# Performance work log

Hardware: AMD Instinct MI355X
Metric: run time of the kernel (lower is better)

Reference implementation:

```python
import jax, jax.numpy as jnp
import numpy as np

NUM_HEADS = 16
HEAD_DIM = 64
HIDDEN = 1024
ROPE_BASE = 10000.0


def _rope_cache(seq_len, dtype):
    inv_freq = 1.0 / (ROPE_BASE ** (jnp.arange(0, HEAD_DIM, 2, dtype=jnp.float32) / HEAD_DIM))
    freqs = jnp.arange(seq_len, dtype=jnp.float32)[:, None] * inv_freq[None, :]  # [S, D/2]
    emb = jnp.concatenate([freqs, freqs], axis=-1)  # [S, D]
    return jnp.cos(emb).astype(dtype), jnp.sin(emb).astype(dtype)


def _rotate_half(x):
    x1, x2 = jnp.split(x, 2, axis=-1)
    return jnp.concatenate([-x2, x1], axis=-1)


def setup_inputs() -> dict:
    key = jax.random.key(0)
    k1, k2, k3 = jax.random.split(key, 3)
    B, S = 1, 4096
    x = jax.random.normal(k1, (B, S, HIDDEN), dtype=jnp.float32)
    w_qkv = jax.random.normal(k2, (3 * HIDDEN, HIDDEN), dtype=jnp.float32) * (1.0 / np.sqrt(HIDDEN))
    w_out = jax.random.normal(k3, (HIDDEN, HIDDEN), dtype=jnp.float32) * (1.0 / np.sqrt(HIDDEN))
    return {"x": x, "w_qkv": w_qkv, "w_out": w_out}


def reference(x, w_qkv, w_out):
    B, S, _ = x.shape
    scale = 1.0 / np.sqrt(HEAD_DIM)
    # fused QKV projection (torch Linear: x @ W^T)
    qkv = jnp.einsum('bsd,ed->bse', x, w_qkv)
    qkv = qkv.reshape(B, S, 3, NUM_HEADS, HEAD_DIM).transpose(2, 0, 3, 1, 4)
    q, k, v = qkv[0], qkv[1], qkv[2]  # [B, H, S, Dh]
    cos, sin = _rope_cache(S, x.dtype)  # [S, Dh]
    cos = cos[None, None]
    sin = sin[None, None]
    q = q * cos + _rotate_half(q) * sin
    k = k * cos + _rotate_half(k) * sin
    scores = jnp.einsum('bhqd,bhkd->bhqk', q, k) * scale  # [B, H, S, S]
    causal = jnp.triu(jnp.ones((S, S), dtype=bool), k=1)
    min_val = jnp.finfo(scores.dtype).min
    scores = jnp.where(causal[None, None], min_val, scores)
    attn = jax.nn.softmax(scores, axis=-1)
    out = jnp.einsum('bhqk,bhkd->bhqd', attn, v)  # [B, H, S, Dh]
    out = out.transpose(0, 2, 1, 3).reshape(B, S, HIDDEN)
    return jnp.einsum('bsd,ed->bse', out, w_out)
```

## Files before the change

kernel.cpp:

```cpp
#include <hip/hip_runtime.h>

#define S_LEN 4096
#define NHEAD 16
#define DHEAD 64
#define HID 1024

typedef float f32x4 __attribute__((ext_vector_type(4)));
typedef float f32x16 __attribute__((ext_vector_type(16)));
typedef unsigned short u16x8 __attribute__((ext_vector_type(8)));
typedef __bf16 bf16x8 __attribute__((ext_vector_type(8)));

__device__ __forceinline__ unsigned short f2bf(float f) {
  union { float f; unsigned u; } x; x.f = f;
  return (unsigned short)((x.u + 0x7FFFu + ((x.u >> 16) & 1u)) >> 16);
}
__device__ __forceinline__ float bf2f(unsigned short u) {
  union { unsigned u; float f; } x; x.u = ((unsigned)u) << 16;
  return x.f;
}
__device__ __forceinline__ f32x4 mfma16(u16x8 a, u16x8 b, f32x4 c) {
  return __builtin_amdgcn_mfma_f32_16x16x32_bf16(
      __builtin_bit_cast(bf16x8, a), __builtin_bit_cast(bf16x8, b), c, 0, 0, 0);
}
__device__ __forceinline__ f32x16 mfma32(u16x8 a, u16x8 b, f32x16 c) {
  return __builtin_amdgcn_mfma_f32_32x32x16_bf16(
      __builtin_bit_cast(bf16x8, a), __builtin_bit_cast(bf16x8, b), c, 0, 0, 0);
}
__device__ __forceinline__ void gload16(const void* g, void* l) {
  __builtin_amdgcn_global_load_lds(
      (const __attribute__((address_space(1))) void*)g,
      (__attribute__((address_space(3))) void*)l, 16, 0, 0);
}
__device__ __forceinline__ void permswap(unsigned& a, unsigned& b) {
#if __has_builtin(__builtin_amdgcn_permlane32_swap)
  typedef unsigned u32x2 __attribute__((ext_vector_type(2)));
  u32x2 r = __builtin_amdgcn_permlane32_swap(a, b, false, false);
  a = r[0]; b = r[1];
#else
  asm volatile("v_permlane32_swap_b32 %0, %1" : "+v"(a), "+v"(b));
#endif
}
__device__ __forceinline__ unsigned cvtpk(float lo, float hi) {
  unsigned r;
  asm("v_cvt_pk_bf16_f32 %0, %1, %2" : "=v"(r) : "v"(lo), "v"(hi));
  return r;
}
__device__ __forceinline__ float fexp2(float x) {
  float r;
  asm("v_exp_f32 %0, %1" : "=v"(r) : "v"(x));
  return r;
}

__global__ void k_cvt_all(const float4* __restrict__ x, const float4* __restrict__ wq,
                          const float4* __restrict__ wo, ushort4* __restrict__ xb,
                          ushort4* __restrict__ wqb, ushort4* __restrict__ wob) {
  int i = blockIdx.x * blockDim.x + threadIdx.x;
  const float4* src; ushort4* dst; int off;
  if (i < 1048576)      { src = x;  dst = xb;  off = i; }
  else if (i < 1835008) { src = wq; dst = wqb; off = i - 1048576; }
  else                  { src = wo; dst = wob; off = i - 1835008; }
  float4 v = src[off];
  ushort4 o;
  o.x = f2bf(v.x); o.y = f2bf(v.y); o.z = f2bf(v.z); o.w = f2bf(v.w);
  dst[off] = o;
}

__global__ void k_rope_split(const unsigned short* __restrict__ qkv,
                             unsigned short* __restrict__ Q,
                             unsigned short* __restrict__ Kf) {
  int s = blockIdx.x;
  int t = threadIdx.x;
  int h = t >> 5, i = t & 31;
  float inv = fexp2(-(float)i * 0.4152410118609203f);
  float ang = (float)s * inv;
  float sn, cs;
  __sincosf(ang, &sn, &cs);
  const unsigned short* row = qkv + (size_t)s * 3072;
  float q1 = bf2f(row[h * 64 + i]);
  float q2 = bf2f(row[h * 64 + i + 32]);
  float k1 = bf2f(row[1024 + h * 64 + i]);
  float k2 = bf2f(row[1024 + h * 64 + i + 32]);
  const float ksc = 0.125f * 1.44269504f;
  size_t qo = ((size_t)h * S_LEN + s) * 64 + i;
  Q[qo]      = f2bf(q1 * cs - q2 * sn);
  Q[qo + 32] = f2bf(q2 * cs + q1 * sn);
  int t32 = s >> 5, kv = s & 31;
  size_t ko = ((((size_t)h * 128 + t32) * 4 + (i >> 4)) * 2 + ((i >> 3) & 1)) * 256 + kv * 8 + (i & 7);
  Kf[ko]        = f2bf((k1 * cs - k2 * sn) * ksc);
  Kf[ko + 1024] = f2bf((k2 * cs + k1 * sn) * ksc);
}

__global__ void k_vt(const unsigned short* __restrict__ qkv,
                     unsigned short* __restrict__ Vf) {
  __shared__ unsigned short tile[64][65];
  int st = blockIdx.x, h = blockIdx.y;
  int t = threadIdx.x;
  int r = t >> 2, c0 = (t & 3) * 16;
  const unsigned short* src = qkv + (size_t)(st * 64 + r) * 3072 + 2048 + h * 64 + c0;
  u16x8 a = *(const u16x8*)src;
  u16x8 b = *(const u16x8*)(src + 8);
#pragma unroll
  for (int j = 0; j < 8; ++j) { tile[r][c0 + j] = a[j]; tile[r][c0 + 8 + j] = b[j]; }
  __syncthreads();
#pragma unroll
  for (int pass = 0; pass < 2; ++pass) {
    int task = t + pass * 256;
    int o = task >> 6, d = task & 63;
    int t32 = st * 2 + (o >> 2), kc = (o >> 1) & 1, hfv = o & 1;
    u16x8 v;
#pragma unroll
    for (int e = 0; e < 8; ++e) v[e] = tile[o * 8 + e][d];
    *(u16x8*)(Vf + (((((size_t)h * 128 + t32) * 2 + kc) * 2 + hfv) * 64 + d) * 8) = v;
  }
}

__device__ __forceinline__ void stc(float* p, float v) { *p = v; }
__device__ __forceinline__ void stc(unsigned short* p, float v) { *p = f2bf(v); }

template <typename OutT>
__global__ __launch_bounds__(256) void gemm_bt(
    const unsigned short* __restrict__ A, const unsigned short* __restrict__ B,
    OutT* __restrict__ C, int M, int N, int K) {
  __shared__ __attribute__((aligned(16))) unsigned short As[2][128][64];
  __shared__ __attribute__((aligned(16))) unsigned short Bs[2][128][64];
  const int tid = threadIdx.x;
  const int w = tid >> 6, lane = tid & 63;
  const int bm = blockIdx.y * 128, bn = blockIdx.x * 128;
  const int wr = w >> 1, wc = w & 1;
  const int l8 = lane >> 3;
  const int c8 = (lane & 7) * 8;
  f32x4 acc[4][4] = {};

  auto stage = [&](int buf, int k0) {
#pragma unroll
    for (int c = 0; c < 4; ++c) {
      int row = w * 32 + c * 8;
      gload16(A + (size_t)(bm + row + l8) * K + k0 + c8, &As[buf][row][0]);
      gload16(B + (size_t)(bn + row + l8) * K + k0 + c8, &Bs[buf][row][0]);
    }
  };

  const int nk = K >> 6;
  stage(0, 0);
  int cur = 0;
  for (int kt = 0; kt < nk; ++kt) {
    __syncthreads();
    if (kt + 1 < nk) stage(cur ^ 1, (kt + 1) << 6);
#pragma unroll
    for (int kk = 0; kk < 2; ++kk) {
      u16x8 af[4], bfr[4];
#pragma unroll
      for (int m = 0; m < 4; ++m)
        af[m] = *(const u16x8*)&As[cur][wr * 64 + m * 16 + (lane & 15)][kk * 32 + (lane >> 4) * 8];
#pragma unroll
      for (int n = 0; n < 4; ++n)
        bfr[n] = *(const u16x8*)&Bs[cur][wc * 64 + n * 16 + (lane & 15)][kk * 32 + (lane >> 4) * 8];
#pragma unroll
      for (int m = 0; m < 4; ++m)
#pragma unroll
        for (int n = 0; n < 4; ++n)
          acc[m][n] = mfma16(af[m], bfr[n], acc[m][n]);
    }
    cur ^= 1;
  }
#pragma unroll
  for (int m = 0; m < 4; ++m) {
    int row = bm + wr * 64 + m * 16 + (lane >> 4) * 4;
#pragma unroll
    for (int n = 0; n < 4; ++n) {
      int col = bn + wc * 64 + n * 16 + (lane & 15);
#pragma unroll
      for (int j = 0; j < 4; ++j) stc(&C[(size_t)(row + j) * N + col], acc[m][n][j]);
    }
  }
}

__device__ __forceinline__ void attn_tile(
    const unsigned short* __restrict__ Q,
    const unsigned short* __restrict__ kfb,
    const unsigned short* __restrict__ vfb,
    unsigned short* __restrict__ O,
    char* eb, int h, int qt, int w, int q31, int hf) {
  const int qb = qt * 128;
  const int qg = qb + w * 32 + q31;

  u16x8 qf[4];
  {
    const unsigned short* qp = Q + ((size_t)h * S_LEN + qg) * 64 + hf * 8;
#pragma unroll
    for (int c = 0; c < 4; ++c) qf[c] = *(const u16x8*)(qp + c * 16);
  }

  f32x16 accA = {}, accB = {};
  float l_own = 0.f;

  const int kOffBase = hf * 256 + q31 * 8;
  const int vOffBase = hf * 512 + q31 * 8;
  const int nst = qt * 4 + w + 1;

  u16x8 ka[4], kb_[4], kc2[4], va[4], vb_[4], vc2[4];
#define LOADK(dst, t)                                                         \
  {                                                                           \
    const unsigned short* p_ = kfb + (size_t)(t) * 2048 + kOffBase;           \
    dst[0] = *(const u16x8*)(p_);                                             \
    dst[1] = *(const u16x8*)(p_ + 512);                                       \
    dst[2] = *(const u16x8*)(p_ + 1024);                                      \
    dst[3] = *(const u16x8*)(p_ + 1536);                                      \
  }
#define LOADV(dst, t)                                                         \
  {                                                                           \
    const unsigned short* p_ = vfb + (size_t)(t) * 2048 + vOffBase;           \
    dst[0] = *(const u16x8*)(p_);                                             \
    dst[1] = *(const u16x8*)(p_ + 256);                                       \
    dst[2] = *(const u16x8*)(p_ + 1024);                                      \
    dst[3] = *(const u16x8*)(p_ + 1280);                                      \
  }
#define STEP(t, kc_, vc_, kn_, vn_)                                           \
  {                                                                           \
    const int tn = ((t) + 2 < nst) ? (t) + 2 : nst - 1;                       \
    LOADK(kn_, tn);                                                           \
    LOADV(vn_, tn);                                                           \
    f32x16 sc = {};                                                           \
    __builtin_amdgcn_s_setprio(1);                                            \
    _Pragma("unroll") for (int c = 0; c < 4; ++c) sc = mfma32(kc_[c], qf[c], sc); \
    __builtin_amdgcn_s_setprio(0);                                            \
    if ((t) == nst - 1) {                     \
      _Pragma("unroll") for (int r = 0; r < 16; ++r) {                        \
        int kvl = (t) * 32 + (r & 3) + 8 * (r >> 2) + 4 * hf;                 \
        if (kvl > qg) sc[r] = -1e30f;                                         \
      }                                                                       \
    }                                                                         \
    float p[16];                                                              \
    _Pragma("unroll") for (int r = 0; r < 16; ++r) p[r] = fexp2(sc[r]);       \
    l_own += (((p[0] + p[1]) + (p[2] + p[3])) + ((p[4] + p[5]) + (p[6] + p[7]))) + \
             (((p[8] + p[9]) + (p[10] + p[11])) + ((p[12] + p[13]) + (p[14] + p[15]))); \
    unsigned dw[8];                                                           \
    _Pragma("unroll") for (int k = 0; k < 8; ++k) dw[k] = cvtpk(p[2 * k], p[2 * k + 1]); \
    __builtin_amdgcn_s_setprio(1);                                            \
    _Pragma("unroll") for (int kc = 0; kc < 2; ++kc) {                        \
      unsigned x0 = dw[4 * kc + 0], x1 = dw[4 * kc + 1];                      \
      unsigned y0 = dw[4 * kc + 2], y1 = dw[4 * kc + 3];                      \
      permswap(x0, y0);                                                       \
      permswap(x1, y1);                                                       \
      union { u16x8 v; unsigned u[4]; } pf;                                   \
      pf.u[0] = x0; pf.u[1] = x1; pf.u[2] = y0; pf.u[3] = y1;                 \
      accA = mfma32(vc_[kc * 2 + 0], pf.v, accA);                             \
      accB = mfma32(vc_[kc * 2 + 1], pf.v, accB);                             \
    }                                                                         \
    __builtin_amdgcn_s_setprio(0);                                            \
  }

  {
    const int t1 = (1 < nst) ? 1 : nst - 1;
    LOADK(ka, 0);
    LOADV(va, 0);
    LOADK(kb_, t1);
    LOADV(vb_, t1);
  }
  int t = 0;
  while (true) {
    STEP(t, ka, va, kc2, vc2);
    if (++t >= nst) break;
    STEP(t, kb_, vb_, ka, va);
    if (++t >= nst) break;
    STEP(t, kc2, vc2, kb_, vb_);
    if (++t >= nst) break;
  }
#undef STEP
#undef LOADK
#undef LOADV

  float l_run;
  {
    unsigned a = __float_as_uint(l_own), b = a;
    permswap(a, b);
    l_run = __uint_as_float(a) + __uint_as_float(b);
  }
  const float inv = 1.0f / l_run;
#pragma unroll
  for (int dblk = 0; dblk < 2; ++dblk) {
#pragma unroll
    for (int tt = 0; tt < 4; ++tt) {
      float a0, a1, a2, a3;
      if (dblk == 0) { a0 = accA[4 * tt]; a1 = accA[4 * tt + 1]; a2 = accA[4 * tt + 2]; a3 = accA[4 * tt + 3]; }
      else           { a0 = accB[4 * tt]; a1 = accB[4 * tt + 1]; a2 = accB[4 * tt + 2]; a3 = accB[4 * tt + 3]; }
      unsigned d0 = cvtpk(a0 * inv, a1 * inv);
      unsigned d1 = cvtpk(a2 * inv, a3 * inv);
      int dbase = dblk * 32 + 8 * tt + 4 * hf;
      int off = (q31 * 128 + dbase * 2) ^ ((q31 & 7) << 4);
      *(uint2*)(eb + off) = make_uint2(d0, d1);
    }
  }
  const int lane = hf * 32 + q31;
#pragma unroll
  for (int pass = 0; pass < 4; ++pass) {
    int q = (lane >> 3) + pass * 8;
    int c8 = lane & 7;
    u16x8 vv = *(const u16x8*)(eb + ((q * 128 + c8 * 16) ^ ((q & 7) << 4)));
    *(u16x8*)(O + (size_t)(qb + w * 32 + q) * HID + h * 64 + c8 * 8) = vv;
  }
}

__global__ __launch_bounds__(256) void flash_attn(
    const unsigned short* __restrict__ Q,
    const unsigned short* __restrict__ Kf,
    const unsigned short* __restrict__ Vf,
    unsigned short* __restrict__ O) {
  __shared__ __attribute__((aligned(16))) unsigned short ebuf[4][2048];
  const int tid = threadIdx.x;
  const int w = tid >> 6, lane = tid & 63;
  const int q31 = lane & 31, hf = lane >> 5;
  const int h = blockIdx.x;
  const int p = blockIdx.y;
  const unsigned short* kfb = Kf + (size_t)h * 128 * 2048;
  const unsigned short* vfb = Vf + (size_t)h * 128 * 2048;
  char* eb = (char*)&ebuf[w][0];
  attn_tile(Q, kfb, vfb, O, eb, h, p, w, q31, hf);
  attn_tile(Q, kfb, vfb, O, eb, h, 31 - p, w, q31, hf);
}

extern "C" void kernel_launch(void* const* d_in, const int* in_sizes, int n_in,
                              void* d_out, int out_size, void* d_ws, size_t ws_size,
                              hipStream_t stream) {
  const float* x = (const float*)d_in[0];
  const float* w_qkv = (const float*)d_in[1];
  const float* w_out = (const float*)d_in[2];
  float* out = (float*)d_out;
  char* ws = (char*)d_ws;

  unsigned short* xb    = (unsigned short*)(ws + 0);
  unsigned short* wqkvb = (unsigned short*)(ws + 8388608);
  unsigned short* woutb = (unsigned short*)(ws + 14680064);
  unsigned short* qkvb  = (unsigned short*)(ws + 16777216);
  unsigned short* Qb    = (unsigned short*)(ws + 41943040);
  unsigned short* Kfb   = (unsigned short*)(ws + 50331648);
  unsigned short* Vfb   = (unsigned short*)(ws + 58720256);
  unsigned short* attnb = (unsigned short*)(ws + 67108864);

  k_cvt_all<<<dim3(8192), dim3(256), 0, stream>>>(
      (const float4*)x, (const float4*)w_qkv, (const float4*)w_out,
      (ushort4*)xb, (ushort4*)wqkvb, (ushort4*)woutb);

  gemm_bt<unsigned short><<<dim3(24, 32), dim3(256), 0, stream>>>(xb, wqkvb, qkvb, 4096, 3072, 1024);

  k_rope_split<<<dim3(4096), dim3(512), 0, stream>>>(qkvb, Qb, Kfb);
  k_vt<<<dim3(64, 16), dim3(256), 0, stream>>>(qkvb, Vfb);

  flash_attn<<<dim3(16, 16), dim3(256), 0, stream>>>(Qb, Kfb, Vfb, attnb);

  gemm_bt<float><<<dim3(8, 32), dim3(256), 0, stream>>>(attnb, woutb, out, 4096, 1024, 1024);
}
```

Baseline: 155.5 us.

## Split paired causal tiles across two wave groups with split-KV partial merge

The attention kernel doubles its block to 512 threads. The first four waves process the short query tile plus the first part of the long tile's KV range. The other four waves process the rest of the long tile's KV range, then merge the first group's partial accumulators and row sums through shared memory before writing the output. The aim is to run the two tiles in parallel instead of sequentially within a block, cutting per-block latency. The cost is extra shared memory (about 66KB more), a block barrier, and higher register pressure under 512-thread launch bounds.

```diff
diff --git a/kernel.cpp b/kernel.cpp
--- a/kernel.cpp
+++ b/kernel.cpp
@@ -175,29 +175,10 @@
   }
 }
 
-__device__ __forceinline__ void attn_tile(
-    const unsigned short* __restrict__ Q,
-    const unsigned short* __restrict__ kfb,
-    const unsigned short* __restrict__ vfb,
-    unsigned short* __restrict__ O,
-    char* eb, int h, int qt, int w, int q31, int hf) {
-  const int qb = qt * 128;
-  const int qg = qb + w * 32 + q31;
-
-  u16x8 qf[4];
-  {
-    const unsigned short* qp = Q + ((size_t)h * S_LEN + qg) * 64 + hf * 8;
-#pragma unroll
-    for (int c = 0; c < 4; ++c) qf[c] = *(const u16x8*)(qp + c * 16);
-  }
-
-  f32x16 accA = {}, accB = {};
-  float l_own = 0.f;
-
-  const int kOffBase = hf * 256 + q31 * 8;
-  const int vOffBase = hf * 512 + q31 * 8;
-  const int nst = qt * 4 + w + 1;
-
+__device__ __forceinline__ void attn_range(
+    const unsigned short* __restrict__ kfb, const unsigned short* __restrict__ vfb,
+    const u16x8* qf, f32x16& accA, f32x16& accB, float& l_own,
+    int t0, int t1, int nst, int qg, int hf, int kOffBase, int vOffBase) {
   u16x8 ka[4], kb_[4], kc2[4], va[4], vb_[4], vc2[4];
 #define LOADK(dst, t)                                                         \
   {                                                                           \
@@ -217,7 +198,7 @@
   }
 #define STEP(t, kc_, vc_, kn_, vn_)                                           \
   {                                                                           \
-    const int tn = ((t) + 2 < nst) ? (t) + 2 : nst - 1;                       \
+    const int tn = ((t) + 2 < t1) ? (t) + 2 : t1 - 1;                         \
     LOADK(kn_, tn);                                                           \
     LOADV(vn_, tn);                                                           \
     f32x16 sc = {};                                                           \
@@ -250,26 +231,30 @@
     __builtin_amdgcn_s_setprio(0);                                            \
   }
 
+  LOADK(ka, t0);
+  LOADV(va, t0);
   {
-    const int t1 = (1 < nst) ? 1 : nst - 1;
-    LOADK(ka, 0);
-    LOADV(va, 0);
-    LOADK(kb_, t1);
-    LOADV(vb_, t1);
-  }
-  int t = 0;
+    const int t1c = (t0 + 1 < t1) ? t0 + 1 : t1 - 1;
+    LOADK(kb_, t1c);
+    LOADV(vb_, t1c);
+  }
+  int t = t0;
   while (true) {
     STEP(t, ka, va, kc2, vc2);
-    if (++t >= nst) break;
+    if (++t >= t1) break;
     STEP(t, kb_, vb_, ka, va);
-    if (++t >= nst) break;
+    if (++t >= t1) break;
     STEP(t, kc2, vc2, kb_, vb_);
-    if (++t >= nst) break;
+    if (++t >= t1) break;
   }
 #undef STEP
 #undef LOADK
 #undef LOADV
-
+}
+
+__device__ __forceinline__ void attn_epilogue(
+    const f32x16& accA, const f32x16& accB, float l_own, char* eb,
+    unsigned short* __restrict__ O, int h, int qb, int wr, int q31, int hf) {
   float l_run;
   {
     unsigned a = __float_as_uint(l_own), b = a;
@@ -297,26 +282,73 @@
     int q = (lane >> 3) + pass * 8;
     int c8 = lane & 7;
     u16x8 vv = *(const u16x8*)(eb + ((q * 128 + c8 * 16) ^ ((q & 7) << 4)));
-    *(u16x8*)(O + (size_t)(qb + w * 32 + q) * HID + h * 64 + c8 * 8) = vv;
-  }
-}
-
-__global__ __launch_bounds__(256) void flash_attn(
+    *(u16x8*)(O + (size_t)(qb + wr * 32 + q) * HID + h * 64 + c8 * 8) = vv;
+  }
+}
+
+__global__ __launch_bounds__(512) void flash_attn(
     const unsigned short* __restrict__ Q,
     const unsigned short* __restrict__ Kf,
     const unsigned short* __restrict__ Vf,
     unsigned short* __restrict__ O) {
-  __shared__ __attribute__((aligned(16))) unsigned short ebuf[4][2048];
+  __shared__ __attribute__((aligned(16))) unsigned short ebuf[8][2048];
+  __shared__ float part[4][64][33];
   const int tid = threadIdx.x;
-  const int w = tid >> 6, lane = tid & 63;
+  const int wv = tid >> 6, lane = tid & 63;
+  const int wr = wv & 3, role = wv >> 2;
   const int q31 = lane & 31, hf = lane >> 5;
   const int h = blockIdx.x;
   const int p = blockIdx.y;
+  const int tileB = 31 - p;
+  const int nstA = 4 * p + wr + 1;
+  const int nstB = 4 * tileB + wr + 1;
+  const int cut = 62 - 4 * p;
+
   const unsigned short* kfb = Kf + (size_t)h * 128 * 2048;
   const unsigned short* vfb = Vf + (size_t)h * 128 * 2048;
-  char* eb = (char*)&ebuf[w][0];
-  attn_tile(Q, kfb, vfb, O, eb, h, p, w, q31, hf);
-  attn_tile(Q, kfb, vfb, O, eb, h, 31 - p, w, q31, hf);
+  const int kOffBase = hf * 256 + q31 * 8;
+  const int vOffBase = hf * 512 + q31 * 8;
+  char* eb = (char*)&ebuf[wv][0];
+
+  const int qgB = tileB * 128 + wr * 32 + q31;
+  u16x8 qfB[4];
+  {
+    const unsigned short* qp = Q + ((size_t)h * S_LEN + qgB) * 64 + hf * 8;
+#pragma unroll
+    for (int c = 0; c < 4; ++c) qfB[c] = *(const u16x8*)(qp + c * 16);
+  }
+
+  if (role == 0) {
+    const int qgA = p * 128 + wr * 32 + q31;
+    u16x8 qfA[4];
+    {
+      const unsigned short* qp = Q + ((size_t)h * S_LEN + qgA) * 64 + hf * 8;
+#pragma unroll
+      for (int c = 0; c < 4; ++c) qfA[c] = *(const u16x8*)(qp + c * 16);
+    }
+    f32x16 accA = {}, accB = {};
+    float l_own = 0.f;
+    attn_range(kfb, vfb, qfA, accA, accB, l_own, 0, nstA, nstA, qgA, hf, kOffBase, vOffBase);
+    attn_epilogue(accA, accB, l_own, eb, O, h, p * 128, wr, q31, hf);
+    f32x16 bA = {}, bB = {};
+    float bl = 0.f;
+    attn_range(kfb, vfb, qfB, bA, bB, bl, 0, cut, nstB, qgB, hf, kOffBase, vOffBase);
+    float* pp = &part[wr][lane][0];
+#pragma unroll
+    for (int r = 0; r < 16; ++r) { pp[r] = bA[r]; pp[16 + r] = bB[r]; }
+    pp[32] = bl;
+    __syncthreads();
+  } else {
+    f32x16 bA = {}, bB = {};
+    float bl = 0.f;
+    attn_range(kfb, vfb, qfB, bA, bB, bl, cut, nstB, nstB, qgB, hf, kOffBase, vOffBase);
+    __syncthreads();
+    const float* pp = &part[wr][lane][0];
+#pragma unroll
+    for (int r = 0; r < 16; ++r) { bA[r] += pp[r]; bB[r] += pp[16 + r]; }
+    bl += pp[32];
+    attn_epilogue(bA, bB, bl, eb, O, h, tileB * 128, wr, q31, hf);
+  }
 }
 
 extern "C" void kernel_launch(void* const* d_in, const int* in_sizes, int n_in,
@@ -346,7 +378,7 @@
   k_rope_split<<<dim3(4096), dim3(512), 0, stream>>>(qkvb, Qb, Kfb);
   k_vt<<<dim3(64, 16), dim3(256), 0, stream>>>(qkvb, Vfb);
 
-  flash_attn<<<dim3(16, 16), dim3(256), 0, stream>>>(Qb, Kfb, Vfb, attnb);
+  flash_attn<<<dim3(16, 16), dim3(512), 0, stream>>>(Qb, Kfb, Vfb, attnb);
 
   gemm_bt<float><<<dim3(8, 32), dim3(256), 0, stream>>>(attnb, woutb, out, 4096, 1024, 1024);
 }
```

After: 142.2 us. 8.5% less time.
